# Kernel tuning notes

Hardware: AMD Instinct MI355X
Metric: run time of the kernel (lower is better)

The kernel has to match this reference:

```python
import jax, jax.numpy as jnp
import numpy as np

DECAY_EPS = 1e-8  # matches F.cosine_similarity eps
DECAY_RATE = 0.999  # buffer decay_rate


def setup_inputs() -> dict:
    key = jax.random.key(0)
    ks = jax.random.split(key, 6)
    B, M, D = 256, 65536, 1024
    return {
        "query": jax.random.normal(ks[0], (B, D), dtype=jnp.float32),
        "mem_keys": jax.random.normal(ks[1], (M, D), dtype=jnp.float32),
        "mem_values": jax.random.normal(ks[2], (M, D), dtype=jnp.float32),
        "importance": jax.random.uniform(ks[3], (M,), dtype=jnp.float32),
        "access_times": jax.random.randint(ks[4], (M,), 0, 1000, dtype=jnp.int32),
        "access_counts": jax.random.randint(ks[5], (M,), 1, 50, dtype=jnp.int32),
        "current_time": 1000,
        "top_k": 8,
    }


def reference(query, mem_keys, mem_values, importance, access_times, access_counts, current_time, top_k):
    # Batched version of AdaptiveMemoryBuffer.retrieve.
    # query: [B, D]; mem_keys/mem_values: [M, D]; importance/access_*: [M]
    qn = query / jnp.maximum(jnp.linalg.norm(query, axis=-1, keepdims=True), DECAY_EPS)
    kn = mem_keys / jnp.maximum(jnp.linalg.norm(mem_keys, axis=-1, keepdims=True), DECAY_EPS)
    sim = qn @ kn.T  # [B, M] cosine similarity

    dt = (current_time - access_times).astype(jnp.float32)           # time since access
    retention = jnp.power(jnp.float32(DECAY_RATE), dt)               # forgetting curve
    freq_bonus = jnp.log1p(access_counts.astype(jnp.float32))        # log(1 + count)
    scores = sim * (retention * importance * freq_bonus)[None, :]    # [B, M]

    top_scores, top_idx = jax.lax.top_k(scores, top_k)                # [B, k]
    weights = jax.nn.softmax(top_scores, axis=-1)                     # [B, k]
    combined = jnp.einsum('bk,bkd->bd', weights, mem_values[top_idx]) # weighted gather
    confidence = weights.max(axis=-1)                                 # [B]
    return combined, confidence
```

## Files before the change

kernel.cpp:

```cpp
#include <hip/hip_runtime.h>
#include <math.h>
#include <float.h>

typedef __attribute__((ext_vector_type(8))) short short8;
typedef __attribute__((ext_vector_type(4))) float f32x4;

namespace {

constexpr int B = 256;
constexpr int M = 65536;
constexpr int D = 1024;
constexpr float DECAY_EPS = 1e-8f;
constexpr float DECAY_RATE = 0.999f;

constexpr int BN = 64;
constexpr int BK = 64;
constexpr int KSTEPS = D / BK;

constexpr int CHUNKS = 8;
constexpr int CHUNK = M / CHUNKS;
constexpr int NCAND = CHUNKS * 8;

__device__ inline ushort f2bf(float f) {
  union { float f; unsigned u; } v; v.f = f;
  unsigned r = v.u + 0x7fffu + ((v.u >> 16) & 1u);
  return (ushort)(r >> 16);
}

__global__ void prep_q_kernel(const float* __restrict__ q, ushort* __restrict__ qnf) {
  const int r = blockIdx.x;
  const int t = threadIdx.x;
  float4 v = reinterpret_cast<const float4*>(q + (size_t)r * D)[t];
  float ss = v.x * v.x + v.y * v.y + v.z * v.z + v.w * v.w;
#pragma unroll
  for (int off = 32; off; off >>= 1) ss += __shfl_down(ss, off, 64);
  __shared__ float red[4];
  if ((t & 63) == 0) red[t >> 6] = ss;
  __syncthreads();
  const float inv = 1.0f / fmaxf(sqrtf(red[0] + red[1] + red[2] + red[3]), DECAY_EPS);
  ushort4 o;
  o.x = f2bf(v.x * inv); o.y = f2bf(v.y * inv);
  o.z = f2bf(v.z * inv); o.w = f2bf(v.w * inv);
  const int k0 = t * 4;
  const int kt = k0 >> 5;
  const int lane_slot = (r & 15) + 16 * ((k0 & 31) >> 3);
  const int j0 = k0 & 7;
  *reinterpret_cast<ushort4*>(qnf + (size_t)(kt * 16 + (r >> 4)) * 512 + lane_slot * 8 + j0) = o;
}

__global__ __launch_bounds__(256) void score_gemm_kernel(
    const ushort* __restrict__ qnf, const float* __restrict__ keys,
    const float* __restrict__ importance, const int* __restrict__ atimes,
    const int* __restrict__ acnts, const int* __restrict__ ctime,
    float* __restrict__ scores) {
  __shared__ alignas(16) ushort Bs[2][BN * BK];
  __shared__ float cscale[BN];

  const int t = threadIdx.x;
  const int lane = t & 63;
  const int w = t >> 6;
  const int jb = blockIdx.x * BN;

  const int rw = t >> 2;
  const int cw = t & 3;
  const float4* kp4 = reinterpret_cast<const float4*>(keys + (size_t)(jb + rw) * D) + cw * 4;

  const int wo0 = rw * BK + (((2 * cw) ^ (rw & 7)) * 8);
  const int wo1 = rw * BK + (((2 * cw + 1) ^ (rw & 7)) * 8);

  int roff[2][4];
#pragma unroll
  for (int ks = 0; ks < 2; ++ks)
#pragma unroll
    for (int nf = 0; nf < 4; ++nf) {
      const int row = nf * 16 + (lane & 15);
      const int slot = ks * 4 + (lane >> 4);
      roff[ks][nf] = row * BK + ((slot ^ (row & 7)) * 8);
    }

  f32x4 acc[4][4];
#pragma unroll
  for (int f = 0; f < 4; ++f)
#pragma unroll
    for (int n = 0; n < 4; ++n) acc[f][n] = (f32x4)(0.0f);

  float kn2 = 0.0f;
  short8 a[2][4];
  float4 bv[4];

  const short8* apbase = reinterpret_cast<const short8*>(qnf);

  auto loadA = [&](int s) {
#pragma unroll
    for (int ks = 0; ks < 2; ++ks)
#pragma unroll
      for (int f = 0; f < 4; ++f)
        a[ks][f] = apbase[(size_t)((2 * s + ks) * 16 + w * 4 + f) * 64 + lane];
  };
  auto loadB = [&](int s) {
#pragma unroll
    for (int i = 0; i < 4; ++i) bv[i] = kp4[s * 16 + i];
  };
  auto stageB = [&](int buf) {
#pragma unroll
    for (int i = 0; i < 4; ++i)
      kn2 += bv[i].x * bv[i].x + bv[i].y * bv[i].y + bv[i].z * bv[i].z + bv[i].w * bv[i].w;
    short8 p0, p1;
    p0[0] = (short)f2bf(bv[0].x); p0[1] = (short)f2bf(bv[0].y);
    p0[2] = (short)f2bf(bv[0].z); p0[3] = (short)f2bf(bv[0].w);
    p0[4] = (short)f2bf(bv[1].x); p0[5] = (short)f2bf(bv[1].y);
    p0[6] = (short)f2bf(bv[1].z); p0[7] = (short)f2bf(bv[1].w);
    p1[0] = (short)f2bf(bv[2].x); p1[1] = (short)f2bf(bv[2].y);
    p1[2] = (short)f2bf(bv[2].z); p1[3] = (short)f2bf(bv[2].w);
    p1[4] = (short)f2bf(bv[3].x); p1[5] = (short)f2bf(bv[3].y);
    p1[6] = (short)f2bf(bv[3].z); p1[7] = (short)f2bf(bv[3].w);
    *reinterpret_cast<short8*>(&Bs[buf][wo0]) = p0;
    *reinterpret_cast<short8*>(&Bs[buf][wo1]) = p1;
  };

  loadB(0);
  stageB(0);
  loadA(0);
  loadB(1);
  __syncthreads();

  for (int s = 0; s < KSTEPS; ++s) {
    const int cur = s & 1;
#pragma unroll
    for (int ks = 0; ks < 2; ++ks) {
      short8 bf[4];
#pragma unroll
      for (int nf = 0; nf < 4; ++nf)
        bf[nf] = *reinterpret_cast<const short8*>(&Bs[cur][roff[ks][nf]]);
#pragma unroll
      for (int f = 0; f < 4; ++f)
#pragma unroll
        for (int nf = 0; nf < 4; ++nf)
          acc[f][nf] = __builtin_amdgcn_mfma_f32_16x16x32_bf16(a[ks][f], bf[nf], acc[f][nf], 0, 0, 0);
    }
    if (s + 1 < KSTEPS) {
      loadA(s + 1);
      stageB(cur ^ 1);
      if (s + 2 < KSTEPS) loadB(s + 2);
    }
    __syncthreads();
  }

  kn2 += __shfl_xor(kn2, 1, 64);
  kn2 += __shfl_xor(kn2, 2, 64);
  if (cw == 0) {
    const int j = jb + rw;
    const float dt = (float)(ctime[0] - atimes[j]);
    const float mult = powf(DECAY_RATE, dt) * importance[j] * log1pf((float)acnts[j]);
    cscale[rw] = mult / fmaxf(sqrtf(kn2), DECAY_EPS);
  }
  __syncthreads();

#pragma unroll
  for (int f = 0; f < 4; ++f) {
    const int row0 = (w * 4 + f) * 16 + ((lane >> 4) << 2);
#pragma unroll
    for (int nf = 0; nf < 4; ++nf) {
      const int col = nf * 16 + (lane & 15);
      const float cs = cscale[col];
#pragma unroll
      for (int rr = 0; rr < 4; ++rr)
        scores[(size_t)(row0 + rr) * M + jb + col] = acc[f][nf][rr] * cs;
    }
  }
}

__global__ __launch_bounds__(256) void topk_partial_kernel(
    const float* __restrict__ scores, int* __restrict__ cand_i) {
  const int b = blockIdx.y;
  const int c = blockIdx.x;
  const int t = threadIdx.x;
  const int lane = t & 63, w = t >> 6;
  const float4* base4 = reinterpret_cast<const float4*>(scores + (size_t)b * M + (size_t)c * CHUNK);

  float s8[8];
  int i8[8];
#pragma unroll
  for (int i = 0; i < 8; ++i) { s8[i] = -FLT_MAX; i8[i] = 0; }

  auto ins = [&](float x, int j) {
    if (x > s8[0]) {
#pragma unroll
      for (int i = 0; i < 8; ++i) {
        const bool up = (i < 7) && (x > s8[i + 1]);
        const float ks = (x > s8[i]) ? x : s8[i];
        const int ki = (x > s8[i]) ? j : i8[i];
        s8[i] = up ? s8[i + 1] : ks;
        i8[i] = up ? i8[i + 1] : ki;
      }
    }
  };

  const int jbase = c * CHUNK;
  for (int it = 0; it < CHUNK / (256 * 4); ++it) {
    const int slot = it * 256 + t;
    const float4 v = base4[slot];
    const int j0 = jbase + slot * 4;
    ins(v.x, j0 + 0);
    ins(v.y, j0 + 1);
    ins(v.z, j0 + 2);
    ins(v.w, j0 + 3);
  }

  __shared__ float ls[2048];
  __shared__ int li[2048];
#pragma unroll
  for (int i = 0; i < 8; ++i) { ls[t * 8 + i] = s8[i]; li[t * 8 + i] = i8[i]; }
  __syncthreads();

  __shared__ float rs4[4];
  __shared__ int rp4[4];
  for (int r = 0; r < 8; ++r) {
    float ms = -FLT_MAX;
    int mp = 0;
#pragma unroll
    for (int i = 0; i < 8; ++i) {
      const float v = ls[i * 256 + t];
      if (v > ms) { ms = v; mp = i * 256 + t; }
    }
#pragma unroll
    for (int off = 32; off; off >>= 1) {
      const float ov = __shfl_xor(ms, off, 64);
      const int op = __shfl_xor(mp, off, 64);
      if (ov > ms) { ms = ov; mp = op; }
    }
    if (lane == 0) { rs4[w] = ms; rp4[w] = mp; }
    __syncthreads();
    if (t == 0) {
      float bs = -FLT_MAX;
      int bp = 0;
#pragma unroll
      for (int i = 0; i < 4; ++i)
        if (rs4[i] > bs) { bs = rs4[i]; bp = rp4[i]; }
      cand_i[((size_t)b * CHUNKS + c) * 8 + r] = li[bp];
      ls[bp] = -FLT_MAX;
    }
    __syncthreads();
  }
}

__global__ __launch_bounds__(512) void rescore_kernel(
    const int* __restrict__ cand_i, const float* __restrict__ query,
    const float* __restrict__ keys, const float* __restrict__ values,
    const float* __restrict__ importance, const int* __restrict__ atimes,
    const int* __restrict__ acnts, const int* __restrict__ ctime,
    float* __restrict__ outc, float* __restrict__ conf) {
  const int b = blockIdx.x;
  const int t = threadIdx.x;
  const int lane = t & 63, w = t >> 6;

  const float4* qv4 = reinterpret_cast<const float4*>(query + (size_t)b * D + lane * 16);
  float4 q0 = qv4[0], q1 = qv4[1], q2 = qv4[2], q3 = qv4[3];
  float ssq = q0.x * q0.x + q0.y * q0.y + q0.z * q0.z + q0.w * q0.w
            + q1.x * q1.x + q1.y * q1.y + q1.z * q1.z + q1.w * q1.w
            + q2.x * q2.x + q2.y * q2.y + q2.z * q2.z + q2.w * q2.w
            + q3.x * q3.x + q3.y * q3.y + q3.z * q3.z + q3.w * q3.w;
#pragma unroll
  for (int off = 32; off; off >>= 1) ssq += __shfl_xor(ssq, off, 64);
  const float qdn = fmaxf(sqrtf(ssq), DECAY_EPS);
  const int ct = ctime[0];

  __shared__ float sc[NCAND];
  __shared__ int sidx[NCAND];

  for (int u = 0; u < 8; ++u) {
    const int c = w * 8 + u;
    const int j = cand_i[(size_t)b * NCAND + c];
    const float4* kv4 = reinterpret_cast<const float4*>(keys + (size_t)j * D + lane * 16);
    const float4 k0 = kv4[0], k1 = kv4[1], k2 = kv4[2], k3 = kv4[3];
    float dd = q0.x * k0.x + q0.y * k0.y + q0.z * k0.z + q0.w * k0.w
             + q1.x * k1.x + q1.y * k1.y + q1.z * k1.z + q1.w * k1.w
             + q2.x * k2.x + q2.y * k2.y + q2.z * k2.z + q2.w * k2.w
             + q3.x * k3.x + q3.y * k3.y + q3.z * k3.z + q3.w * k3.w;
    float nn = k0.x * k0.x + k0.y * k0.y + k0.z * k0.z + k0.w * k0.w
             + k1.x * k1.x + k1.y * k1.y + k1.z * k1.z + k1.w * k1.w
             + k2.x * k2.x + k2.y * k2.y + k2.z * k2.z + k2.w * k2.w
             + k3.x * k3.x + k3.y * k3.y + k3.z * k3.z + k3.w * k3.w;
#pragma unroll
    for (int off = 32; off; off >>= 1) {
      dd += __shfl_xor(dd, off, 64);
      nn += __shfl_xor(nn, off, 64);
    }
    if (lane == 0) {
      const float dtv = (float)(ct - atimes[j]);
      const float mult = powf(DECAY_RATE, dtv) * importance[j] * log1pf((float)acnts[j]);
      sc[c] = dd / (qdn * fmaxf(sqrtf(nn), DECAY_EPS)) * mult;
      sidx[c] = j;
    }
  }
  __syncthreads();

  __shared__ float w8s[8];
  __shared__ int g8[8];
  __shared__ float confv;
  __shared__ float tls[8];
  __shared__ int tli[8];
  if (w == 0) {
    float myv = sc[lane];
    for (int r = 0; r < 8; ++r) {
      float m = myv;
      int mi = lane;
#pragma unroll
      for (int off = 32; off; off >>= 1) {
        const float ov = __shfl_xor(m, off, 64);
        const int oi = __shfl_xor(mi, off, 64);
        if (ov > m || (ov == m && oi < mi)) { m = ov; mi = oi; }
      }
      if (lane == 0) { tls[r] = m; tli[r] = mi; }
      if (lane == mi) myv = -FLT_MAX;
    }
    if (lane == 0) {
      const float mx = tls[0];
      float e[8];
      float z = 0.0f;
#pragma unroll
      for (int r = 0; r < 8; ++r) { e[r] = expf(tls[r] - mx); z += e[r]; }
      const float invz = 1.0f / z;
#pragma unroll
      for (int r = 0; r < 8; ++r) { w8s[r] = e[r] * invz; g8[r] = sidx[tli[r]]; }
      confv = w8s[0];
    }
  }
  __syncthreads();

  float2 acc = make_float2(0.0f, 0.0f);
#pragma unroll
  for (int k = 0; k < 8; ++k) {
    const float wk = w8s[k];
    const float2 v = *reinterpret_cast<const float2*>(values + (size_t)g8[k] * D + 2 * t);
    acc.x = fmaf(wk, v.x, acc.x);
    acc.y = fmaf(wk, v.y, acc.y);
  }
  *reinterpret_cast<float2*>(outc + (size_t)b * D + 2 * t) = acc;
  if (t == 0) conf[b] = confv;
}

}

extern "C" void kernel_launch(void* const* d_in, const int* in_sizes, int n_in,
                              void* d_out, int out_size, void* d_ws, size_t ws_size,
                              hipStream_t stream) {
  const float* query = (const float*)d_in[0];
  const float* keys = (const float*)d_in[1];
  const float* values = (const float*)d_in[2];
  const float* importance = (const float*)d_in[3];
  const int* atimes = (const int*)d_in[4];
  const int* acnts = (const int*)d_in[5];
  const int* ctime = (const int*)d_in[6];

  float* out = (float*)d_out;
  ushort* qnf = (ushort*)d_ws;
  float* scores = (float*)((char*)d_ws + (size_t)B * D * sizeof(ushort));
  int* cand = (int*)(scores + (size_t)B * M);

  prep_q_kernel<<<B, 256, 0, stream>>>(query, qnf);
  score_gemm_kernel<<<M / BN, 256, 0, stream>>>(qnf, keys, importance, atimes,
                                                acnts, ctime, scores);
  dim3 gA(CHUNKS, B);
  topk_partial_kernel<<<gA, 256, 0, stream>>>(scores, cand);
  rescore_kernel<<<B, 512, 0, stream>>>(cand, query, keys, values, importance,
                                        atimes, acnts, ctime, out, out + (size_t)B * D);
}
```

Baseline: 150.3 us.

## Stage fp32 key tiles via direct global-to-LDS loads, convert to bf16 at fragment read

The score GEMM now copies raw fp32 key tiles straight into shared memory with the async global_load_lds builtin instead of loading them into registers, converting to bf16 and storing. Conversion to bf16 and the key-norm accumulation move to the point where each wave reads its MFMA fragments, using a new XOR swizzle. The aim is to cut register pressure and VGPR round trips, allowing a launch_bounds occupancy hint of 3. The cost is doubled LDS footprint and redundant per-wave bf16 conversion of every B fragment.

```diff
diff --git a/kernel.cpp b/kernel.cpp
--- a/kernel.cpp
+++ b/kernel.cpp
@@ -1,4 +1,5 @@
 #include <hip/hip_runtime.h>
+#include <hip/hip_bf16.h>
 #include <math.h>
 #include <float.h>
 
@@ -25,6 +26,18 @@
   union { float f; unsigned u; } v; v.f = f;
   unsigned r = v.u + 0x7fffu + ((v.u >> 16) & 1u);
   return (ushort)(r >> 16);
+}
+
+__device__ inline short bfs(float f) {
+  __hip_bfloat16 h = __float2bfloat16(f);
+  return *reinterpret_cast<short*>(&h);
+}
+
+__device__ inline short8 pack8(float4 u, float4 v) {
+  short8 r;
+  r[0] = bfs(u.x); r[1] = bfs(u.y); r[2] = bfs(u.z); r[3] = bfs(u.w);
+  r[4] = bfs(v.x); r[5] = bfs(v.y); r[6] = bfs(v.z); r[7] = bfs(v.w);
+  return r;
 }
 
 __global__ void prep_q_kernel(const float* __restrict__ q, ushort* __restrict__ qnf) {
@@ -48,35 +61,36 @@
   *reinterpret_cast<ushort4*>(qnf + (size_t)(kt * 16 + (r >> 4)) * 512 + lane_slot * 8 + j0) = o;
 }
 
-__global__ __launch_bounds__(256) void score_gemm_kernel(
+__global__ __launch_bounds__(256, 3) void score_gemm_kernel(
     const ushort* __restrict__ qnf, const float* __restrict__ keys,
     const float* __restrict__ importance, const int* __restrict__ atimes,
     const int* __restrict__ acnts, const int* __restrict__ ctime,
     float* __restrict__ scores) {
-  __shared__ alignas(16) ushort Bs[2][BN * BK];
+  __shared__ alignas(16) float Bs[2][BN * BK];
   __shared__ float cscale[BN];
 
   const int t = threadIdx.x;
   const int lane = t & 63;
   const int w = t >> 6;
+  const int h = lane >> 4;
+  const int q = lane & 15;
   const int jb = blockIdx.x * BN;
 
-  const int rw = t >> 2;
-  const int cw = t & 3;
-  const float4* kp4 = reinterpret_cast<const float4*>(keys + (size_t)(jb + rw) * D) + cw * 4;
-
-  const int wo0 = rw * BK + (((2 * cw) ^ (rw & 7)) * 8);
-  const int wo1 = rw * BK + (((2 * cw + 1) ^ (rw & 7)) * 8);
-
-  int roff[2][4];
-#pragma unroll
-  for (int ks = 0; ks < 2; ++ks)
-#pragma unroll
-    for (int nf = 0; nf < 4; ++nf) {
-      const int row = nf * 16 + (lane & 15);
-      const int slot = ks * 4 + (lane >> 4);
-      roff[ks][nf] = row * BK + ((slot ^ (row & 7)) * 8);
-    }
+  const int swz_w = (q ^ (h << 1) ^ (w & 1)) * 4;
+  const float* kbase = keys + (size_t)(jb + w * 4 + h) * D + swz_w;
+
+  auto stage = [&](int s, int buf) {
+#pragma unroll
+    for (int i = 0; i < 4; ++i) {
+      const float* gp = kbase + (size_t)i * 16 * D + s * BK;
+      float* lp = &Bs[buf][i * 1024 + w * 256];
+      __builtin_amdgcn_global_load_lds(
+          (const __attribute__((address_space(1))) void*)gp,
+          (__attribute__((address_space(3))) void*)lp, 16, 0, 0);
+    }
+  };
+
+  const int mrd = ((q & 3) << 1) | ((q >> 2) & 1);
 
   f32x4 acc[4][4];
 #pragma unroll
@@ -84,84 +98,69 @@
 #pragma unroll
     for (int n = 0; n < 4; ++n) acc[f][n] = (f32x4)(0.0f);
 
-  float kn2 = 0.0f;
-  short8 a[2][4];
-  float4 bv[4];
+  float nrm = 0.0f;
+
+  stage(0, 0);
+  __syncthreads();
 
   const short8* apbase = reinterpret_cast<const short8*>(qnf);
-
-  auto loadA = [&](int s) {
-#pragma unroll
-    for (int ks = 0; ks < 2; ++ks)
-#pragma unroll
-      for (int f = 0; f < 4; ++f)
-        a[ks][f] = apbase[(size_t)((2 * s + ks) * 16 + w * 4 + f) * 64 + lane];
-  };
-  auto loadB = [&](int s) {
-#pragma unroll
-    for (int i = 0; i < 4; ++i) bv[i] = kp4[s * 16 + i];
-  };
-  auto stageB = [&](int buf) {
-#pragma unroll
-    for (int i = 0; i < 4; ++i)
-      kn2 += bv[i].x * bv[i].x + bv[i].y * bv[i].y + bv[i].z * bv[i].z + bv[i].w * bv[i].w;
-    short8 p0, p1;
-    p0[0] = (short)f2bf(bv[0].x); p0[1] = (short)f2bf(bv[0].y);
-    p0[2] = (short)f2bf(bv[0].z); p0[3] = (short)f2bf(bv[0].w);
-    p0[4] = (short)f2bf(bv[1].x); p0[5] = (short)f2bf(bv[1].y);
-    p0[6] = (short)f2bf(bv[1].z); p0[7] = (short)f2bf(bv[1].w);
-    p1[0] = (short)f2bf(bv[2].x); p1[1] = (short)f2bf(bv[2].y);
-    p1[2] = (short)f2bf(bv[2].z); p1[3] = (short)f2bf(bv[2].w);
-    p1[4] = (short)f2bf(bv[3].x); p1[5] = (short)f2bf(bv[3].y);
-    p1[6] = (short)f2bf(bv[3].z); p1[7] = (short)f2bf(bv[3].w);
-    *reinterpret_cast<short8*>(&Bs[buf][wo0]) = p0;
-    *reinterpret_cast<short8*>(&Bs[buf][wo1]) = p1;
-  };
-
-  loadB(0);
-  stageB(0);
-  loadA(0);
-  loadB(1);
-  __syncthreads();
 
   for (int s = 0; s < KSTEPS; ++s) {
     const int cur = s & 1;
+    if (s + 1 < KSTEPS) stage(s + 1, cur ^ 1);
+
+    short8 a[2][4];
+    {
+      const short8* ap = apbase + (size_t)(2 * s * 16 + w * 4) * 64 + lane;
+#pragma unroll
+      for (int ks = 0; ks < 2; ++ks)
+#pragma unroll
+        for (int f = 0; f < 4; ++f) a[ks][f] = ap[(ks * 16 + f) * 64];
+    }
+
 #pragma unroll
     for (int ks = 0; ks < 2; ++ks) {
-      short8 bf[4];
-#pragma unroll
-      for (int nf = 0; nf < 4; ++nf)
-        bf[nf] = *reinterpret_cast<const short8*>(&Bs[cur][roff[ks][nf]]);
+      const int cbase = ks * 8 + h * 2;
+      short8 bfrag[4];
+#pragma unroll
+      for (int nf = 0; nf < 4; ++nf) {
+        const int ro = (nf * 16 + q) * 64;
+        const float4 lo = *reinterpret_cast<const float4*>(
+            &Bs[cur][ro + ((cbase ^ mrd) << 2)]);
+        const float4 hi = *reinterpret_cast<const float4*>(
+            &Bs[cur][ro + (((cbase + 1) ^ mrd) << 2)]);
+        if (nf == w) {
+          nrm += lo.x * lo.x + lo.y * lo.y + lo.z * lo.z + lo.w * lo.w
+               + hi.x * hi.x + hi.y * hi.y + hi.z * hi.z + hi.w * hi.w;
+        }
+        bfrag[nf] = pack8(lo, hi);
+      }
 #pragma unroll
       for (int f = 0; f < 4; ++f)
 #pragma unroll
         for (int nf = 0; nf < 4; ++nf)
-          acc[f][nf] = __builtin_amdgcn_mfma_f32_16x16x32_bf16(a[ks][f], bf[nf], acc[f][nf], 0, 0, 0);
-    }
-    if (s + 1 < KSTEPS) {
-      loadA(s + 1);
-      stageB(cur ^ 1);
-      if (s + 2 < KSTEPS) loadB(s + 2);
+          acc[f][nf] = __builtin_amdgcn_mfma_f32_16x16x32_bf16(
+              a[ks][f], bfrag[nf], acc[f][nf], 0, 0, 0);
     }
     __syncthreads();
   }
 
-  kn2 += __shfl_xor(kn2, 1, 64);
-  kn2 += __shfl_xor(kn2, 2, 64);
-  if (cw == 0) {
-    const int j = jb + rw;
+  nrm += __shfl_xor(nrm, 16, 64);
+  nrm += __shfl_xor(nrm, 32, 64);
+  if (lane < 16) {
+    const int j = jb + w * 16 + lane;
     const float dt = (float)(ctime[0] - atimes[j]);
     const float mult = powf(DECAY_RATE, dt) * importance[j] * log1pf((float)acnts[j]);
-    cscale[rw] = mult / fmaxf(sqrtf(kn2), DECAY_EPS);
+    cscale[w * 16 + lane] = mult / fmaxf(sqrtf(nrm), DECAY_EPS);
   }
   __syncthreads();
 
 #pragma unroll
   for (int f = 0; f < 4; ++f) {
-    const int row0 = (w * 4 + f) * 16 + ((lane >> 4) << 2);
+    const int row0 = (w * 4 + f) * 16 + (h << 2);
 #pragma unroll
     for (int nf = 0; nf < 4; ++nf) {
-      const int col = nf * 16 + (lane & 15);
+      const int col = nf * 16 + q;
       const float cs = cscale[col];
 #pragma unroll
       for (int rr = 0; rr < 4; ++rr)
```

Measured after the change: 156.7 us. +4.3%, slower.
